# Optimization experiments

Measured on AMD Instinct MI355X. Metric: run time of the kernel, lower is better.

The kernel has to match this reference:

```python
import jax, jax.numpy as jnp
import numpy as np


def fake_quant(x):
    # Per-tensor symmetric int8 fake quantization with straight-through estimator.
    scale = jnp.maximum(jnp.max(jnp.abs(x)) / 127.0, 1e-8)
    q = jnp.clip(jnp.round(x / scale), -128.0, 127.0) * scale
    return x + jax.lax.stop_gradient(q - x)


def setup_inputs() -> dict:
    key = jax.random.key(0)
    k = jax.random.split(key, 6)
    B, R, M0, M1, OUT = 8192, 64, 64, 64, 4096
    return {
        "x0": jax.random.normal(k[0], (B, M0), dtype=jnp.float32),
        "x1": jax.random.normal(k[1], (B, M1), dtype=jnp.float32),
        "f0": jax.random.normal(k[2], (M0, R), dtype=jnp.float32) * 0.1,
        "f1": jax.random.normal(k[3], (M1, R), dtype=jnp.float32) * 0.1,
        "f2": jax.random.normal(k[4], (OUT, R), dtype=jnp.float32) * 0.1,
        "bias": jnp.full((OUT,), 0.1, dtype=jnp.float32),
    }


def reference(x0, x1, f0, f1, f2, bias):
    # CP factor matmul chain with elementwise (Hadamard) fusion over modes
    out = (x0 @ fake_quant(f0)) * (x1 @ fake_quant(f1))  # [B, R]
    out = out @ fake_quant(f2).T                          # [B, OUT]
    out = fake_quant(out + bias)
    return jax.nn.relu(out)
```

## Files before the change

### kernel.cpp

```cpp
#include <hip/hip_runtime.h>
#include <math.h>

#define NB   8192
#define NR   64
#define NOUT 4096

typedef __attribute__((ext_vector_type(8))) short bf16x8;
typedef __attribute__((ext_vector_type(4))) float f32x4;


static constexpr size_t OFF_PF2  = 256;
static constexpr size_t OFF_BMAX = 2048;
static constexpr size_t OFF_FC2  = 16384;
static constexpr size_t OFF_FTH  = OFF_FC2 + 256 * 2048;
static constexpr size_t OFF_FTL  = OFF_FTH + (size_t)512 * 2048 * 2;

__device__ __forceinline__ float wave_max(float v) {
#pragma unroll
  for (int off = 32; off > 0; off >>= 1) v = fmaxf(v, __shfl_down(v, off));
  return v;
}

__device__ __forceinline__ unsigned short f2bf(float f) {
  unsigned u = __float_as_uint(f);
  unsigned r = u + 0x7fff + ((u >> 16) & 1);
  return (unsigned short)(r >> 16);
}
__device__ __forceinline__ float bf2f(unsigned short h) {
  return __uint_as_float(((unsigned)h) << 16);
}
__device__ __forceinline__ float qcode(float x, float sinv) {
  return fminf(fmaxf(rintf(x * sinv), -128.0f), 127.0f);
}

__device__ __forceinline__ int ft_idx(int row, int k) {
  return (row >> 4) * 1024 + (k >> 5) * 512 +
         ((row & 15) + (((k & 31) >> 3) << 4)) * 8 + (k & 7);
}

__device__ __forceinline__ void split8(float4 a, float4 b, bf16x8& h, bf16x8& lo) {
  float v[8] = {a.x, a.y, a.z, a.w, b.x, b.y, b.z, b.w};
#pragma unroll
  for (int j = 0; j < 8; ++j) {
    unsigned short hh = f2bf(v[j]);
    h[j] = (short)hh;
    lo[j] = (short)f2bf(v[j] - bf2f(hh));
  }
}

__global__ __launch_bounds__(256) void absmax_f2(
    const float* __restrict__ f2, float* __restrict__ pf2) {
  __shared__ float wred[4];
  int tid = threadIdx.x;
  float4 v = ((const float4*)f2)[blockIdx.x * 256 + tid];
  float a = fmaxf(fmaxf(fabsf(v.x), fabsf(v.y)), fmaxf(fabsf(v.z), fabsf(v.w)));
  a = wave_max(a);
  if ((tid & 63) == 0) wred[tid >> 6] = a;
  __syncthreads();
  if (tid == 0)
    pf2[blockIdx.x] = fmaxf(fmaxf(wred[0], wred[1]), fmaxf(wred[2], wred[3]));
}

__global__ __launch_bounds__(256) void prep_f2(
    const float* __restrict__ f2, const float* __restrict__ pf2,
    float* __restrict__ slots_f, unsigned short* __restrict__ fc2) {
  __shared__ float wred[4];
  int tid = threadIdx.x, bid = blockIdx.x;
  float a = pf2[tid];
  a = wave_max(a);
  if ((tid & 63) == 0) wred[tid >> 6] = a;
  __syncthreads();
  float am = fmaxf(fmaxf(wred[0], wred[1]), fmaxf(wred[2], wred[3]));
  float s2 = fmaxf(am * (1.0f / 127.0f), 1e-8f);
  if (bid == 0 && tid == 0) slots_f[2] = s2;
  float sinv = 1.0f / s2;
  int i4 = bid * 256 + tid;
  int e = i4 * 4, m = e >> 6, r0 = e & 63;
  float4 v = ((const float4*)f2)[i4];
  unsigned short c0 = f2bf(qcode(v.x, sinv)), c1 = f2bf(qcode(v.y, sinv));
  unsigned short cc2 = f2bf(qcode(v.z, sinv)), c3 = f2bf(qcode(v.w, sinv));
  uint2 p;
  p.x = (unsigned)c0 | ((unsigned)c1 << 16);
  p.y = (unsigned)cc2 | ((unsigned)c3 << 16);
  *(uint2*)(fc2 + ft_idx(m, r0)) = p;
}

__global__ __launch_bounds__(256) void stage1_fused(
    const float* __restrict__ x0, const float* __restrict__ x1,
    const float* __restrict__ f0, const float* __restrict__ f1,
    unsigned short* __restrict__ fth, unsigned short* __restrict__ ftl) {
  __shared__ float wred0[4], wred1[4];
  __shared__ unsigned short c0s[4096], c1s[4096];
  int tid = threadIdx.x;

  float a0 = 0.0f, a1 = 0.0f;
#pragma unroll
  for (int i = 0; i < 4; ++i) {
    float4 v0 = ((const float4*)f0)[tid + i * 256];
    float4 v1 = ((const float4*)f1)[tid + i * 256];
    a0 = fmaxf(a0, fmaxf(fmaxf(fabsf(v0.x), fabsf(v0.y)),
                         fmaxf(fabsf(v0.z), fabsf(v0.w))));
    a1 = fmaxf(a1, fmaxf(fmaxf(fabsf(v1.x), fabsf(v1.y)),
                         fmaxf(fabsf(v1.z), fabsf(v1.w))));
  }
  a0 = wave_max(a0);
  a1 = wave_max(a1);
  if ((tid & 63) == 0) { wred0[tid >> 6] = a0; wred1[tid >> 6] = a1; }
  __syncthreads();
  float am0 = fmaxf(fmaxf(wred0[0], wred0[1]), fmaxf(wred0[2], wred0[3]));
  float am1 = fmaxf(fmaxf(wred1[0], wred1[1]), fmaxf(wred1[2], wred1[3]));
  float s0 = fmaxf(am0 * (1.0f / 127.0f), 1e-8f);
  float s1 = fmaxf(am1 * (1.0f / 127.0f), 1e-8f);
  float sinv0 = 1.0f / s0, sinv1 = 1.0f / s1;

  int m = tid >> 2, rb = (tid & 3) * 16;
#pragma unroll
  for (int i = 0; i < 4; ++i) {
    float4 v0 = ((const float4*)f0)[tid * 4 + i];
    float4 v1 = ((const float4*)f1)[tid * 4 + i];
    float w0[4] = {v0.x, v0.y, v0.z, v0.w};
    float w1[4] = {v1.x, v1.y, v1.z, v1.w};
#pragma unroll
    for (int j = 0; j < 4; ++j) {
      int r = rb + i * 4 + j;
      c0s[ft_idx(r, m)] = f2bf(qcode(w0[j], sinv0));
      c1s[ft_idx(r, m)] = f2bf(qcode(w1[j], sinv1));
    }
  }
  __syncthreads();

  int l = tid & 63, nf = tid >> 6;
  int b0 = blockIdx.x * 16;
  int row = b0 + (l & 15), kb = (l >> 4) * 8;
  const float* p0 = x0 + (size_t)row * 64 + kb;
  const float* p1 = x1 + (size_t)row * 64 + kb;
  bf16x8 a0h0, a0l0, a0h1, a0l1, a1h0, a1l0, a1h1, a1l1;
  split8(*(const float4*)p0, *(const float4*)(p0 + 4), a0h0, a0l0);
  split8(*(const float4*)(p0 + 32), *(const float4*)(p0 + 36), a0h1, a0l1);
  split8(*(const float4*)p1, *(const float4*)(p1 + 4), a1h0, a1l0);
  split8(*(const float4*)(p1 + 32), *(const float4*)(p1 + 36), a1h1, a1l1);

  bf16x8 b0a = *(const bf16x8*)(c0s + nf * 1024 + l * 8);
  bf16x8 b0b = *(const bf16x8*)(c0s + nf * 1024 + l * 8 + 512);
  bf16x8 b1a = *(const bf16x8*)(c1s + nf * 1024 + l * 8);
  bf16x8 b1b = *(const bf16x8*)(c1s + nf * 1024 + l * 8 + 512);

  f32x4 acc0 = {}, acc1 = {};
  acc0 = __builtin_amdgcn_mfma_f32_16x16x32_bf16(a0h0, b0a, acc0, 0, 0, 0);
  acc0 = __builtin_amdgcn_mfma_f32_16x16x32_bf16(a0l0, b0a, acc0, 0, 0, 0);
  acc0 = __builtin_amdgcn_mfma_f32_16x16x32_bf16(a0h1, b0b, acc0, 0, 0, 0);
  acc0 = __builtin_amdgcn_mfma_f32_16x16x32_bf16(a0l1, b0b, acc0, 0, 0, 0);
  acc1 = __builtin_amdgcn_mfma_f32_16x16x32_bf16(a1h0, b1a, acc1, 0, 0, 0);
  acc1 = __builtin_amdgcn_mfma_f32_16x16x32_bf16(a1l0, b1a, acc1, 0, 0, 0);
  acc1 = __builtin_amdgcn_mfma_f32_16x16x32_bf16(a1h1, b1b, acc1, 0, 0, 0);
  acc1 = __builtin_amdgcn_mfma_f32_16x16x32_bf16(a1l1, b1b, acc1, 0, 0, 0);

  float s01 = s0 * s1;
#pragma unroll
  for (int j = 0; j < 4; ++j) {
    float tv = s01 * acc0[j] * acc1[j];
    int row_in = (l >> 4) * 4 + j;
    int r = nf * 16 + (l & 15);
    int idx = blockIdx.x * 1024 + (r >> 5) * 512 +
              (row_in + (((r & 31) >> 3) << 4)) * 8 + (r & 7);
    unsigned short h = f2bf(tv);
    fth[idx] = h;
    ftl[idx] = f2bf(tv - bf2f(h));
  }
}

template <int MODE>
__global__ __launch_bounds__(256) void stage2(
    const unsigned short* __restrict__ fth, const unsigned short* __restrict__ ftl,
    const unsigned short* __restrict__ fc2, const float* __restrict__ bias,
    const float* __restrict__ slots_f, float* __restrict__ bmax,
    float* __restrict__ out) {
  __shared__ float wred[4];
  int flat = blockIdx.x;
  int xcd = flat & 7, local = flat >> 3;
  int mt = xcd * 4 + (local >> 6);
  int nt = local & 63;
  int tid = threadIdx.x;
  int wid = tid >> 6, l = tid & 63;
  int m0 = mt * 256 + wid * 64;
  int n0 = nt * 64;
  int mt0 = m0 >> 4, nt0 = n0 >> 4;
  float s2 = slots_f[2];

  bf16x8 bfr[4][2];
#pragma unroll
  for (int nf = 0; nf < 4; ++nf) {
    int bb = (nt0 + nf) * 1024 + l * 8;
    bfr[nf][0] = *(const bf16x8*)(fc2 + bb);
    bfr[nf][1] = *(const bf16x8*)(fc2 + bb + 512);
  }

  f32x4 acc[4][4] = {};
#pragma unroll
  for (int mf = 0; mf < 4; ++mf) {
    int ab = (mt0 + mf) * 1024 + l * 8;
    bf16x8 ah0 = *(const bf16x8*)(fth + ab), ah1 = *(const bf16x8*)(fth + ab + 512);
    bf16x8 al0 = *(const bf16x8*)(ftl + ab), al1 = *(const bf16x8*)(ftl + ab + 512);
#pragma unroll
    for (int nf = 0; nf < 4; ++nf) {
      acc[mf][nf] = __builtin_amdgcn_mfma_f32_16x16x32_bf16(ah0, bfr[nf][0], acc[mf][nf], 0, 0, 0);
      acc[mf][nf] = __builtin_amdgcn_mfma_f32_16x16x32_bf16(al0, bfr[nf][0], acc[mf][nf], 0, 0, 0);
      acc[mf][nf] = __builtin_amdgcn_mfma_f32_16x16x32_bf16(ah1, bfr[nf][1], acc[mf][nf], 0, 0, 0);
      acc[mf][nf] = __builtin_amdgcn_mfma_f32_16x16x32_bf16(al1, bfr[nf][1], acc[mf][nf], 0, 0, 0);
    }
  }

  float bs[4];
#pragma unroll
  for (int nf = 0; nf < 4; ++nf) bs[nf] = bias[n0 + nf * 16 + (l & 15)];

  if (MODE == 0) {
    float m = 0.0f;
#pragma unroll
    for (int mf = 0; mf < 4; ++mf)
#pragma unroll
      for (int nf = 0; nf < 4; ++nf)
#pragma unroll
        for (int j = 0; j < 4; ++j)
          m = fmaxf(m, fabsf(s2 * acc[mf][nf][j] + bs[nf]));
    m = wave_max(m);
    if ((tid & 63) == 0) wred[tid >> 6] = m;
    __syncthreads();
    if (tid == 0) {
      bmax[flat] = fmaxf(fmaxf(wred[0], wred[1]), fmaxf(wred[2], wred[3]));
    }
  } else {
    float sY = slots_f[3];
    float inv = 1.0f / sY;
#pragma unroll
    for (int mf = 0; mf < 4; ++mf) {
      int r0 = m0 + mf * 16 + (l >> 4) * 4;
#pragma unroll
      for (int nf = 0; nf < 4; ++nf) {
        int c = n0 + nf * 16 + (l & 15);
#pragma unroll
        for (int j = 0; j < 4; ++j) {
          float v = s2 * acc[mf][nf][j] + bs[nf];
          float q = fminf(fmaxf(rintf(v * inv), -128.0f), 127.0f) * sY;
          out[(size_t)(r0 + j) * NOUT + c] = fmaxf(q, 0.0f);
        }
      }
    }
  }
}

__global__ __launch_bounds__(256) void reduce_bmax(
    const float* __restrict__ bmax, float* __restrict__ slots_f) {
  __shared__ float wred[4];
  int tid = threadIdx.x;
  float m = 0.0f;
#pragma unroll
  for (int i = 0; i < 8; ++i) m = fmaxf(m, bmax[tid + i * 256]);
  m = wave_max(m);
  if ((tid & 63) == 0) wred[tid >> 6] = m;
  __syncthreads();
  if (tid == 0) {
    float mm = fmaxf(fmaxf(wred[0], wred[1]), fmaxf(wred[2], wred[3]));
    slots_f[3] = fmaxf(mm * (1.0f / 127.0f), 1e-8f);
  }
}

extern "C" void kernel_launch(void* const* d_in, const int* in_sizes, int n_in,
                              void* d_out, int out_size, void* d_ws,
                              size_t ws_size, hipStream_t stream) {
  (void)in_sizes; (void)n_in; (void)out_size; (void)ws_size;
  const float* x0 = (const float*)d_in[0];
  const float* x1 = (const float*)d_in[1];
  const float* f0 = (const float*)d_in[2];
  const float* f1 = (const float*)d_in[3];
  const float* f2 = (const float*)d_in[4];
  const float* bias = (const float*)d_in[5];
  float* out = (float*)d_out;

  char* ws = (char*)d_ws;
  float* slots_f = (float*)ws;
  float* pf2  = (float*)(ws + OFF_PF2);
  float* bmax = (float*)(ws + OFF_BMAX);
  unsigned short* fc2 = (unsigned short*)(ws + OFF_FC2);
  unsigned short* fth = (unsigned short*)(ws + OFF_FTH);
  unsigned short* ftl = (unsigned short*)(ws + OFF_FTL);

  absmax_f2<<<256, 256, 0, stream>>>(f2, pf2);
  prep_f2<<<256, 256, 0, stream>>>(f2, pf2, slots_f, fc2);
  stage1_fused<<<512, 256, 0, stream>>>(x0, x1, f0, f1, fth, ftl);
  stage2<0><<<2048, 256, 0, stream>>>(fth, ftl, fc2, bias, slots_f, bmax,
                                      nullptr);
  reduce_bmax<<<1, 256, 0, stream>>>(bmax, slots_f);
  stage2<1><<<2048, 256, 0, stream>>>(fth, ftl, fc2, bias, slots_f, nullptr,
                                      out);
}
```

Baseline: 170.7 us.

## Fold f2 prep and scale reductions into prep and GEMM kernels

The f2 absmax pass now runs as extra blocks of the stage-1 kernel. The separate f2 quantize/pack kernel and the bmax reduce kernel are removed. Each stage2 block re-reduces the partial maxima itself and quantizes its f2 fragments straight from fp32 into registers, so six launches become three and the fc2 workspace is no longer needed. The cost is redundant per-block reduction of pf2 (and of bmax in mode 1), plus uncoalesced fp32 f2 reads and quantization repeated in every GEMM block.

New measurement: 192.3 us. 12.7% more time.

```diff
diff --git a/kernel.cpp b/kernel.cpp
--- a/kernel.cpp
+++ b/kernel.cpp
@@ -11,9 +11,8 @@
 
 static constexpr size_t OFF_PF2  = 256;
 static constexpr size_t OFF_BMAX = 2048;
-static constexpr size_t OFF_FC2  = 16384;
-static constexpr size_t OFF_FTH  = OFF_FC2 + 256 * 2048;
-static constexpr size_t OFF_FTL  = OFF_FTH + (size_t)512 * 2048 * 2;
+static constexpr size_t OFF_FTH  = 16384;
+static constexpr size_t OFF_FTL  = OFF_FTH + (size_t)512 * 2048;
 
 __device__ __forceinline__ float wave_max(float v) {
 #pragma unroll
@@ -48,50 +47,34 @@
   }
 }
 
-__global__ __launch_bounds__(256) void absmax_f2(
-    const float* __restrict__ f2, float* __restrict__ pf2) {
-  __shared__ float wred[4];
-  int tid = threadIdx.x;
-  float4 v = ((const float4*)f2)[blockIdx.x * 256 + tid];
-  float a = fmaxf(fmaxf(fabsf(v.x), fabsf(v.y)), fmaxf(fabsf(v.z), fabsf(v.w)));
-  a = wave_max(a);
-  if ((tid & 63) == 0) wred[tid >> 6] = a;
-  __syncthreads();
-  if (tid == 0)
-    pf2[blockIdx.x] = fmaxf(fmaxf(wred[0], wred[1]), fmaxf(wred[2], wred[3]));
-}
-
-__global__ __launch_bounds__(256) void prep_f2(
-    const float* __restrict__ f2, const float* __restrict__ pf2,
-    float* __restrict__ slots_f, unsigned short* __restrict__ fc2) {
-  __shared__ float wred[4];
-  int tid = threadIdx.x, bid = blockIdx.x;
-  float a = pf2[tid];
-  a = wave_max(a);
-  if ((tid & 63) == 0) wred[tid >> 6] = a;
-  __syncthreads();
-  float am = fmaxf(fmaxf(wred[0], wred[1]), fmaxf(wred[2], wred[3]));
-  float s2 = fmaxf(am * (1.0f / 127.0f), 1e-8f);
-  if (bid == 0 && tid == 0) slots_f[2] = s2;
-  float sinv = 1.0f / s2;
-  int i4 = bid * 256 + tid;
-  int e = i4 * 4, m = e >> 6, r0 = e & 63;
-  float4 v = ((const float4*)f2)[i4];
-  unsigned short c0 = f2bf(qcode(v.x, sinv)), c1 = f2bf(qcode(v.y, sinv));
-  unsigned short cc2 = f2bf(qcode(v.z, sinv)), c3 = f2bf(qcode(v.w, sinv));
-  uint2 p;
-  p.x = (unsigned)c0 | ((unsigned)c1 << 16);
-  p.y = (unsigned)cc2 | ((unsigned)c3 << 16);
-  *(uint2*)(fc2 + ft_idx(m, r0)) = p;
-}
-
-__global__ __launch_bounds__(256) void stage1_fused(
+__device__ __forceinline__ bf16x8 pack8q(float4 a, float4 b, float sinv) {
+  float v[8] = {a.x, a.y, a.z, a.w, b.x, b.y, b.z, b.w};
+  bf16x8 c;
+#pragma unroll
+  for (int j = 0; j < 8; ++j) c[j] = (short)f2bf(qcode(v[j], sinv));
+  return c;
+}
+
+__global__ __launch_bounds__(256) void prep_all(
     const float* __restrict__ x0, const float* __restrict__ x1,
     const float* __restrict__ f0, const float* __restrict__ f1,
+    const float* __restrict__ f2, float* __restrict__ pf2,
     unsigned short* __restrict__ fth, unsigned short* __restrict__ ftl) {
   __shared__ float wred0[4], wred1[4];
   __shared__ unsigned short c0s[4096], c1s[4096];
   int tid = threadIdx.x;
+
+  if (blockIdx.x >= 512) {
+    int bid = blockIdx.x - 512;
+    float4 v = ((const float4*)f2)[bid * 256 + tid];
+    float a = fmaxf(fmaxf(fabsf(v.x), fabsf(v.y)), fmaxf(fabsf(v.z), fabsf(v.w)));
+    a = wave_max(a);
+    if ((tid & 63) == 0) wred0[tid >> 6] = a;
+    __syncthreads();
+    if (tid == 0)
+      pf2[bid] = fmaxf(fmaxf(wred0[0], wred0[1]), fmaxf(wred0[2], wred0[3]));
+    return;
+  }
 
   float a0 = 0.0f, a1 = 0.0f;
 #pragma unroll
@@ -172,27 +155,49 @@
 template <int MODE>
 __global__ __launch_bounds__(256) void stage2(
     const unsigned short* __restrict__ fth, const unsigned short* __restrict__ ftl,
-    const unsigned short* __restrict__ fc2, const float* __restrict__ bias,
-    const float* __restrict__ slots_f, float* __restrict__ bmax,
+    const float* __restrict__ f2, const float* __restrict__ bias,
+    const float* __restrict__ pf2, float* __restrict__ bmax,
     float* __restrict__ out) {
-  __shared__ float wred[4];
+  __shared__ float wred[4], wred2[4];
+  int tid = threadIdx.x;
+
+  float a = pf2[tid];
+  a = wave_max(a);
+  if ((tid & 63) == 0) wred[tid >> 6] = a;
+  float ym = 0.0f;
+  if (MODE == 1) {
+#pragma unroll
+    for (int i = 0; i < 8; ++i) ym = fmaxf(ym, bmax[tid + i * 256]);
+    ym = wave_max(ym);
+    if ((tid & 63) == 0) wred2[tid >> 6] = ym;
+  }
+  __syncthreads();
+  float am = fmaxf(fmaxf(wred[0], wred[1]), fmaxf(wred[2], wred[3]));
+  float s2 = fmaxf(am * (1.0f / 127.0f), 1e-8f);
+  float sinv2 = 1.0f / s2;
+  float sY = 1.0f;
+  if (MODE == 1) {
+    float mm = fmaxf(fmaxf(wred2[0], wred2[1]), fmaxf(wred2[2], wred2[3]));
+    sY = fmaxf(mm * (1.0f / 127.0f), 1e-8f);
+  }
+
   int flat = blockIdx.x;
   int xcd = flat & 7, local = flat >> 3;
   int mt = xcd * 4 + (local >> 6);
   int nt = local & 63;
-  int tid = threadIdx.x;
   int wid = tid >> 6, l = tid & 63;
   int m0 = mt * 256 + wid * 64;
   int n0 = nt * 64;
-  int mt0 = m0 >> 4, nt0 = n0 >> 4;
-  float s2 = slots_f[2];
+  int mt0 = m0 >> 4;
+  int kb = (l >> 4) * 8;
 
   bf16x8 bfr[4][2];
 #pragma unroll
   for (int nf = 0; nf < 4; ++nf) {
-    int bb = (nt0 + nf) * 1024 + l * 8;
-    bfr[nf][0] = *(const bf16x8*)(fc2 + bb);
-    bfr[nf][1] = *(const bf16x8*)(fc2 + bb + 512);
+    int row = n0 + nf * 16 + (l & 15);
+    const float* p = f2 + (size_t)row * 64 + kb;
+    bfr[nf][0] = pack8q(*(const float4*)p, *(const float4*)(p + 4), sinv2);
+    bfr[nf][1] = pack8q(*(const float4*)(p + 32), *(const float4*)(p + 36), sinv2);
   }
 
   f32x4 acc[4][4] = {};
@@ -226,11 +231,9 @@
     m = wave_max(m);
     if ((tid & 63) == 0) wred[tid >> 6] = m;
     __syncthreads();
-    if (tid == 0) {
+    if (tid == 0)
       bmax[flat] = fmaxf(fmaxf(wred[0], wred[1]), fmaxf(wred[2], wred[3]));
-    }
   } else {
-    float sY = slots_f[3];
     float inv = 1.0f / sY;
 #pragma unroll
     for (int mf = 0; mf < 4; ++mf) {
@@ -246,22 +249,6 @@
         }
       }
     }
-  }
-}
-
-__global__ __launch_bounds__(256) void reduce_bmax(
-    const float* __restrict__ bmax, float* __restrict__ slots_f) {
-  __shared__ float wred[4];
-  int tid = threadIdx.x;
-  float m = 0.0f;
-#pragma unroll
-  for (int i = 0; i < 8; ++i) m = fmaxf(m, bmax[tid + i * 256]);
-  m = wave_max(m);
-  if ((tid & 63) == 0) wred[tid >> 6] = m;
-  __syncthreads();
-  if (tid == 0) {
-    float mm = fmaxf(fmaxf(wred[0], wred[1]), fmaxf(wred[2], wred[3]));
-    slots_f[3] = fmaxf(mm * (1.0f / 127.0f), 1e-8f);
   }
 }
 
@@ -278,19 +265,12 @@
   float* out = (float*)d_out;
 
   char* ws = (char*)d_ws;
-  float* slots_f = (float*)ws;
   float* pf2  = (float*)(ws + OFF_PF2);
   float* bmax = (float*)(ws + OFF_BMAX);
-  unsigned short* fc2 = (unsigned short*)(ws + OFF_FC2);
   unsigned short* fth = (unsigned short*)(ws + OFF_FTH);
   unsigned short* ftl = (unsigned short*)(ws + OFF_FTL);
 
-  absmax_f2<<<256, 256, 0, stream>>>(f2, pf2);
-  prep_f2<<<256, 256, 0, stream>>>(f2, pf2, slots_f, fc2);
-  stage1_fused<<<512, 256, 0, stream>>>(x0, x1, f0, f1, fth, ftl);
-  stage2<0><<<2048, 256, 0, stream>>>(fth, ftl, fc2, bias, slots_f, bmax,
-                                      nullptr);
-  reduce_bmax<<<1, 256, 0, stream>>>(bmax, slots_f);
-  stage2<1><<<2048, 256, 0, stream>>>(fth, ftl, fc2, bias, slots_f, nullptr,
-                                      out);
-}
+  prep_all<<<768, 256, 0, stream>>>(x0, x1, f0, f1, f2, pf2, fth, ftl);
+  stage2<0><<<2048, 256, 0, stream>>>(fth, ftl, f2, bias, pf2, bmax, nullptr);
+  stage2<1><<<2048, 256, 0, stream>>>(fth, ftl, f2, bias, pf2, bmax, out);
+}
```
